# Kernel optimization log

Measured on AMD Instinct MI355X. Metric: run time of the kernel, lower is better.

The kernel has to match this reference:

```python
import jax, jax.numpy as jnp
import numpy as np

N = 50000      # nodes
E = 800000     # edges (before self-loops)
F_IN = 256
H = 4          # heads
C1 = 128
C2 = 64
NCLS = 50
NEG_SLOPE = 0.2


def setup_inputs() -> dict:
    key = jax.random.key(0)
    ks = jax.random.split(key, 12)
    x = jax.random.normal(ks[0], (N, F_IN), dtype=jnp.float32)
    edge_index = jax.random.randint(ks[1], (2, E), 0, N, dtype=jnp.int32)
    s1 = 1.0 / np.sqrt(F_IN)
    s2 = 1.0 / np.sqrt(H * C1)
    s3 = 1.0 / np.sqrt(H * C2)
    return {
        "x": x,
        "edge_index": edge_index,
        "W1": jax.random.normal(ks[2], (F_IN, H * C1), dtype=jnp.float32) * s1,
        "a_src1": jax.random.normal(ks[3], (H, C1), dtype=jnp.float32) * s2,
        "a_dst1": jax.random.normal(ks[4], (H, C1), dtype=jnp.float32) * s2,
        "b1": jnp.zeros((H * C1,), dtype=jnp.float32),
        "W2": jax.random.normal(ks[5], (H * C1, H * C2), dtype=jnp.float32) * s2,
        "a_src2": jax.random.normal(ks[6], (H, C2), dtype=jnp.float32) * s3,
        "a_dst2": jax.random.normal(ks[7], (H, C2), dtype=jnp.float32) * s3,
        "b2": jnp.zeros((H * C2,), dtype=jnp.float32),
        "Wf": jax.random.normal(ks[8], (H * C2, NCLS), dtype=jnp.float32) * s3,
        "bf": jnp.zeros((NCLS,), dtype=jnp.float32),
    }


def _gat_conv(x, src, dst, W, a_src, a_dst, b, heads, ch):
    # h: [N, H, C] transformed features
    h = (x @ W).reshape(N, heads, ch)
    # per-node attention halves (standard GAT decomposition, avoids per-edge d-dim gather for scores)
    asrc = jnp.sum(h * a_src[None], axis=-1)  # [N, H]
    adst = jnp.sum(h * a_dst[None], axis=-1)  # [N, H]
    e = jax.nn.leaky_relu(asrc[src] + adst[dst], NEG_SLOPE)  # [E, H]
    # softmax over edges sharing the same destination node
    m = jax.ops.segment_max(e, dst, num_segments=N)          # [N, H]
    ex = jnp.exp(e - m[dst])
    denom = jax.ops.segment_sum(ex, dst, num_segments=N)     # [N, H]
    alpha = ex / (denom[dst] + 1e-16)                        # [E, H]
    msg = h[src] * alpha[:, :, None]                         # [E, H, C]
    out = jax.ops.segment_sum(msg, dst, num_segments=N)      # [N, H, C]
    return out.reshape(N, heads * ch) + b


def reference(x, edge_index, W1, a_src1, a_dst1, b1, W2, a_src2, a_dst2, b2, Wf, bf):
    # PyG GATConv adds self-loops by default
    loops = jnp.arange(N, dtype=edge_index.dtype)
    src = jnp.concatenate([edge_index[0], loops])
    dst = jnp.concatenate([edge_index[1], loops])
    h = _gat_conv(x, src, dst, W1, a_src1, a_dst1, b1, H, C1)
    h = jax.nn.elu(h)
    # F.dropout is identity in eval mode
    h = _gat_conv(h, src, dst, W2, a_src2, a_dst2, b2, H, C2)
    h = jax.nn.elu(h)
    return h @ Wf + bf
```

## Files before the change

kernel.cpp:

```cpp
#include <hip/hip_runtime.h>
#include <hip/hip_bf16.h>
#include <cmath>

#define NN 50000
#define EE 800000
#define ET 850000
#define HH 4
#define CC1 128
#define CC2 64
#define FIN 256
#define NCLS 50

typedef __attribute__((ext_vector_type(8))) short   short8;
typedef __attribute__((ext_vector_type(8))) unsigned short ushort8;
typedef __attribute__((ext_vector_type(4))) unsigned short ushortx4;
typedef __attribute__((ext_vector_type(4))) float   floatx4;

__device__ __forceinline__ unsigned short f2bf(float f) {
    union { float f; unsigned int u; } x; x.f = f;
    unsigned int lsb = (x.u >> 16) & 1u;
    x.u += 0x7fffu + lsb;
    return (unsigned short)(x.u >> 16);
}
__device__ __forceinline__ float bf2f(unsigned short b) {
    union { unsigned int u; float f; } x; x.u = ((unsigned int)b) << 16;
    return x.f;
}

typedef const __attribute__((address_space(1))) unsigned int* glds_gp_t;
typedef __attribute__((address_space(3))) unsigned int* glds_lp_t;
__device__ __forceinline__ void glds16(const void* g, void* l) {
    __builtin_amdgcn_global_load_lds((glds_gp_t)g, (glds_lp_t)l, 16, 0, 0);
}

__global__ __launch_bounds__(256) void cast_bf16(
    const float* __restrict__ in, unsigned short* __restrict__ out, int n4)
{
    int t = blockIdx.x * blockDim.x + threadIdx.x;
    if (t >= n4) return;
    float4 v = *(const float4*)(in + 4 * (size_t)t);
    unsigned short r0 = f2bf(v.x), r1 = f2bf(v.y), r2 = f2bf(v.z), r3 = f2bf(v.w);
    unsigned int lo = (unsigned int)r0 | ((unsigned int)r1 << 16);
    unsigned int hi = (unsigned int)r2 | ((unsigned int)r3 << 16);
    *(uint2*)(out + 4 * (size_t)t) = make_uint2(lo, hi);
}

__global__ __launch_bounds__(256) void transpose_cast(
    const float* __restrict__ W, unsigned short* __restrict__ Wt, int K, int N)
{
    int t = blockIdx.x * blockDim.x + threadIdx.x;
    if (t >= K * N) return;
    int n = t / K, k = t - n * K;
    Wt[t] = f2bf(W[(size_t)k * N + n]);
}

__global__ __launch_bounds__(256) void transpose_cast_pad(
    const float* __restrict__ W, unsigned short* __restrict__ Wt,
    int K, int N, int Npad)
{
    int t = blockIdx.x * blockDim.x + threadIdx.x;
    if (t >= K * Npad) return;
    int n = t / K, k = t - n * K;
    Wt[t] = (n < N) ? f2bf(W[(size_t)k * N + n]) : (unsigned short)0;
}

__global__ __launch_bounds__(256) void gemm_bf16_v2(
    const unsigned short* __restrict__ A,
    const unsigned short* __restrict__ Bt,
    unsigned short* __restrict__ C,
    int M, int N, int K)
{
    __shared__ unsigned short As[128 * 32];
    __shared__ unsigned short Bs[128 * 32];
    int tid = threadIdx.x, wave = tid >> 6, lane = tid & 63;
    int wm = (wave >> 1) * 64, wn = (wave & 1) * 64;
    int row0 = blockIdx.x * 128, col0 = blockIdx.y * 128;
    int lm = lane & 15, lq = lane >> 4, kq = lq * 8;
    floatx4 acc[4][4] = {};

    int srow = wave * 32 + (lane >> 2);
    int skk  = (lane & 3) * 8;
    int gra0 = row0 + srow;      if (gra0 >= M) gra0 = M - 1;
    int gra1 = row0 + srow + 16; if (gra1 >= M) gra1 = M - 1;
    const unsigned short* ga0 = A + (size_t)gra0 * K + skk;
    const unsigned short* ga1 = A + (size_t)gra1 * K + skk;
    const unsigned short* gb0 = Bt + (size_t)(col0 + srow) * K + skk;
    const unsigned short* gb1 = Bt + (size_t)(col0 + srow + 16) * K + skk;
    unsigned short* la0 = &As[(wave * 32) * 32];
    unsigned short* la1 = &As[(wave * 32 + 16) * 32];
    unsigned short* lb0 = &Bs[(wave * 32) * 32];
    unsigned short* lb1 = &Bs[(wave * 32 + 16) * 32];

    for (int k0 = 0; k0 < K; k0 += 32) {
        __syncthreads();
        glds16(ga0 + k0, la0);
        glds16(ga1 + k0, la1);
        glds16(gb0 + k0, lb0);
        glds16(gb1 + k0, lb1);
        __syncthreads();

        short8 af[4], bfr[4];
        #pragma unroll
        for (int mt = 0; mt < 4; ++mt)
            af[mt] = *(const short8*)&As[(wm + mt * 16 + lm) * 32 + kq];
        #pragma unroll
        for (int nt = 0; nt < 4; ++nt)
            bfr[nt] = *(const short8*)&Bs[(wn + nt * 16 + lm) * 32 + kq];
        #pragma unroll
        for (int mt = 0; mt < 4; ++mt)
            #pragma unroll
            for (int nt = 0; nt < 4; ++nt)
                acc[mt][nt] = __builtin_amdgcn_mfma_f32_16x16x32_bf16(
                    af[mt], bfr[nt], acc[mt][nt], 0, 0, 0);
    }

    #pragma unroll
    for (int mt = 0; mt < 4; ++mt) {
        int rbase = row0 + wm + mt * 16 + lq * 4;
        #pragma unroll
        for (int nt = 0; nt < 4; ++nt) {
            int c = col0 + wn + nt * 16 + lm;
            #pragma unroll
            for (int r = 0; r < 4; ++r) {
                int gr = rbase + r;
                if (gr < M) C[(size_t)gr * N + c] = f2bf(acc[mt][nt][r]);
            }
        }
    }
}

__global__ __launch_bounds__(128) void gemm_final(
    const unsigned short* __restrict__ A,
    const unsigned short* __restrict__ Bt,
    const float* __restrict__ bias,
    float* __restrict__ out, int M)
{
    __shared__ unsigned short As[128 * 40];
    __shared__ unsigned short Bs[64 * 40];
    int tid = threadIdx.x, wave = tid >> 6, lane = tid & 63;
    int row0 = blockIdx.x * 128;
    int lm = lane & 15, lq = lane >> 4, kq = lq * 8;
    floatx4 acc[4][4] = {};

    for (int k0 = 0; k0 < 256; k0 += 32) {
        int gr = row0 + tid; if (gr >= M) gr = M - 1;
        const unsigned short* ap = A + (size_t)gr * 256 + k0;
        ushort8 a0 = *(const ushort8*)ap;
        ushort8 a1 = *(const ushort8*)(ap + 8);
        ushort8 a2 = *(const ushort8*)(ap + 16);
        ushort8 a3 = *(const ushort8*)(ap + 24);
        const unsigned short* bp = Bt + (size_t)(tid >> 1) * 256 + k0 + (tid & 1) * 16;
        ushort8 b0 = *(const ushort8*)bp;
        ushort8 b1 = *(const ushort8*)(bp + 8);
        __syncthreads();
        *(ushort8*)&As[tid * 40 + 0]  = a0;
        *(ushort8*)&As[tid * 40 + 8]  = a1;
        *(ushort8*)&As[tid * 40 + 16] = a2;
        *(ushort8*)&As[tid * 40 + 24] = a3;
        *(ushort8*)&Bs[(tid >> 1) * 40 + (tid & 1) * 16]     = b0;
        *(ushort8*)&Bs[(tid >> 1) * 40 + (tid & 1) * 16 + 8] = b1;
        __syncthreads();

        short8 af[4], bfr[4];
        #pragma unroll
        for (int mt = 0; mt < 4; ++mt)
            af[mt] = *(const short8*)&As[(wave * 64 + mt * 16 + lm) * 40 + kq];
        #pragma unroll
        for (int nt = 0; nt < 4; ++nt)
            bfr[nt] = *(const short8*)&Bs[(nt * 16 + lm) * 40 + kq];
        #pragma unroll
        for (int mt = 0; mt < 4; ++mt)
            #pragma unroll
            for (int nt = 0; nt < 4; ++nt)
                acc[mt][nt] = __builtin_amdgcn_mfma_f32_16x16x32_bf16(
                    af[mt], bfr[nt], acc[mt][nt], 0, 0, 0);
    }

    #pragma unroll
    for (int mt = 0; mt < 4; ++mt) {
        int rbase = row0 + wave * 64 + mt * 16 + lq * 4;
        #pragma unroll
        for (int nt = 0; nt < 4; ++nt) {
            int c = nt * 16 + lm;
            if (c >= NCLS) continue;
            float bv = bias[c];
            #pragma unroll
            for (int r = 0; r < 4; ++r) {
                int gr = rbase + r;
                if (gr < M) out[(size_t)gr * NCLS + c] = acc[mt][nt][r] + bv;
            }
        }
    }
}

template<int C>
__global__ __launch_bounds__(256) void attn_scores2(
    const unsigned short* __restrict__ h, const float* __restrict__ a_src,
    const float* __restrict__ a_dst, float* __restrict__ asrc,
    float* __restrict__ adst)
{
    constexpr int HC = HH * C;
    constexpr int CPL = HC / 64;
    int wave = threadIdx.x >> 6;
    int lane = threadIdx.x & 63;
    int n = blockIdx.x * 4 + wave;
    if (n >= NN) return;
    int c0 = lane * CPL;
    int head = c0 / C;
    const unsigned short* hp = h + (size_t)n * HC + c0;
    float hv[CPL];
    if (CPL == 8) {
        ushort8 u = *(const ushort8*)hp;
        #pragma unroll
        for (int c = 0; c < 8; ++c) hv[c] = bf2f(u[c]);
    } else {
        ushortx4 u = *(const ushortx4*)hp;
        #pragma unroll
        for (int c = 0; c < 4; ++c) hv[c] = bf2f(u[c]);
    }
    float s1 = 0.f, s2 = 0.f;
    #pragma unroll
    for (int c = 0; c < CPL; ++c) {
        s1 += hv[c] * a_src[c0 + c];
        s2 += hv[c] * a_dst[c0 + c];
    }
    #pragma unroll
    for (int o = 8; o > 0; o >>= 1) {
        s1 += __shfl_xor(s1, o, 64);
        s2 += __shfl_xor(s2, o, 64);
    }
    if ((lane & 15) == 0) {
        asrc[n * HH + head] = s1;
        adst[n * HH + head] = s2;
    }
}

__global__ void edge_histogram(const int* __restrict__ ei, int* __restrict__ deg)
{
    int t = blockIdx.x * blockDim.x + threadIdx.x;
    if (t >= ET) return;
    int dst = (t < EE) ? ei[EE + t] : (t - EE);
    atomicAdd(&deg[dst], 1);
}

__global__ __launch_bounds__(256) void scan_reduce(
    const int* __restrict__ deg, int* __restrict__ partials)
{
    int i0 = blockIdx.x * 2048 + threadIdx.x * 8;
    int s = 0;
    #pragma unroll
    for (int k = 0; k < 8; ++k) { int i = i0 + k; s += (i < NN) ? deg[i] : 0; }
    #pragma unroll
    for (int o = 32; o > 0; o >>= 1) s += __shfl_xor(s, o, 64);
    __shared__ int ws[4];
    int lane = threadIdx.x & 63, wid = threadIdx.x >> 6;
    if (lane == 0) ws[wid] = s;
    __syncthreads();
    if (threadIdx.x == 0) partials[blockIdx.x] = ws[0] + ws[1] + ws[2] + ws[3];
}

__global__ __launch_bounds__(64) void scan_partials(int* __restrict__ partials, int nb)
{
    int lane = threadIdx.x;
    int v = (lane < nb) ? partials[lane] : 0;
    int s = v;
    #pragma unroll
    for (int o = 1; o < 64; o <<= 1) {
        int t = __shfl_up(s, o, 64);
        if (lane >= o) s += t;
    }
    if (lane < nb) partials[lane] = s - v;
}

__global__ __launch_bounds__(256) void scan_apply(
    const int* __restrict__ deg, const int* __restrict__ partials,
    int* __restrict__ off, int* __restrict__ pos)
{
    int i0 = blockIdx.x * 2048 + threadIdx.x * 8;
    int v[8]; int s = 0;
    #pragma unroll
    for (int k = 0; k < 8; ++k) {
        int i = i0 + k;
        v[k] = (i < NN) ? deg[i] : 0;
        s += v[k];
    }
    int lane = threadIdx.x & 63, wid = threadIdx.x >> 6;
    int sc = s;
    #pragma unroll
    for (int o = 1; o < 64; o <<= 1) {
        int t = __shfl_up(sc, o, 64);
        if (lane >= o) sc += t;
    }
    __shared__ int ws[4];
    if (lane == 63) ws[wid] = sc;
    __syncthreads();
    int woff = partials[blockIdx.x];
    for (int w = 0; w < wid; ++w) woff += ws[w];
    int excl = woff + sc - s;
    #pragma unroll
    for (int k = 0; k < 8; ++k) {
        int i = i0 + k;
        if (i < NN) { off[i] = excl; pos[i] = excl; }
        excl += v[k];
    }
    if (blockIdx.x == 0 && threadIdx.x == 0) off[NN] = ET;
}

__global__ void edge_scatter(const int* __restrict__ ei,
                             int* __restrict__ pos, int* __restrict__ csr_src)
{
    int t = blockIdx.x * blockDim.x + threadIdx.x;
    if (t >= ET) return;
    int src, dst;
    if (t < EE) { src = ei[t]; dst = ei[EE + t]; }
    else        { src = t - EE; dst = t - EE; }
    int p = atomicAdd(&pos[dst], 1);
    csr_src[p] = src;
}

template<int C>
__global__ __launch_bounds__(256) void aggregate5(
    const unsigned short* __restrict__ h, const int* __restrict__ off,
    const int* __restrict__ csr_src, const float* __restrict__ asrc,
    const float* __restrict__ adst, const float* __restrict__ bias,
    unsigned short* __restrict__ outb)
{
    constexpr int HC = HH * C;
    constexpr int LPE = HC / 8;
    constexpr int EPW = 64 / LPE;
    __shared__ float exlds_all[4][64 * HH];
    int wave = threadIdx.x >> 6;
    int lane = threadIdx.x & 63;
    int n = blockIdx.x * 4 + wave;
    if (n >= NN) return;
    float* exlds = exlds_all[wave];
    int el  = (EPW == 1) ? 0 : (lane >> 5);
    int lel = (EPW == 1) ? lane : (lane & 31);
    int coff = lel * 8;
    int hl = coff / C;

    int start = off[n], end = off[n + 1];
    float4 advv = *(const float4*)(adst + (size_t)n * HH);
    float dh0 = 0.f, dh1 = 0.f, dh2 = 0.f, dh3 = 0.f;
    float acc[8] = {0.f, 0.f, 0.f, 0.f, 0.f, 0.f, 0.f, 0.f};

    for (int cb = start; cb < end; cb += 64) {
        int eidx = cb + lane;
        bool valid = eidx < end;
        int s_lane = csr_src[valid ? eidx : end - 1];
        float4 t = *(const float4*)(asrc + (size_t)s_lane * HH);
        float e0 = t.x + advv.x; e0 = e0 > 0.f ? e0 : 0.2f * e0;
        float e1 = t.y + advv.y; e1 = e1 > 0.f ? e1 : 0.2f * e1;
        float e2 = t.z + advv.z; e2 = e2 > 0.f ? e2 : 0.2f * e2;
        float e3 = t.w + advv.w; e3 = e3 > 0.f ? e3 : 0.2f * e3;
        float x0 = valid ? __expf(e0) : 0.f;
        float x1 = valid ? __expf(e1) : 0.f;
        float x2 = valid ? __expf(e2) : 0.f;
        float x3 = valid ? __expf(e3) : 0.f;
        dh0 += x0; dh1 += x1; dh2 += x2; dh3 += x3;
        *(float4*)&exlds[lane * 4] = make_float4(x0, x1, x2, x3);

        int cnt = end - cb; if (cnt > 64) cnt = 64;
        int jmax = (cnt + 4 * EPW - 1) & ~(4 * EPW - 1);
        for (int jj = 0; jj < jmax; jj += 4 * EPW) {
            int sidx[4]; float xs[4]; ushort8 uv[4];
            #pragma unroll
            for (int u = 0; u < 4; ++u) {
                int e_lo = jj + u * EPW;
                if (EPW == 1) {
                    sidx[u] = __builtin_amdgcn_readlane(s_lane, e_lo);
                } else {
                    int sa = __builtin_amdgcn_readlane(s_lane, e_lo);
                    int sb = __builtin_amdgcn_readlane(s_lane, e_lo + 1);
                    sidx[u] = el ? sb : sa;
                }
                xs[u] = exlds[(e_lo + el) * 4 + hl];
                uv[u] = *(const ushort8*)(h + (size_t)sidx[u] * HC + coff);
            }
            #pragma unroll
            for (int u = 0; u < 4; ++u)
                #pragma unroll
                for (int c = 0; c < 8; ++c)
                    acc[c] += xs[u] * bf2f(uv[u][c]);
        }
    }

    #pragma unroll
    for (int o = 32; o > 0; o >>= 1) {
        dh0 += __shfl_xor(dh0, o, 64);
        dh1 += __shfl_xor(dh1, o, 64);
        dh2 += __shfl_xor(dh2, o, 64);
        dh3 += __shfl_xor(dh3, o, 64);
    }
    if (EPW == 2) {
        #pragma unroll
        for (int c = 0; c < 8; ++c)
            acc[c] += __shfl_xor(acc[c], 32, 64);
    }
    float d = (hl == 0) ? dh0 : (hl == 1) ? dh1 : (hl == 2) ? dh2 : dh3;
    float inv = 1.f / (d + 1e-16f);
    if (el == 0) {
        float4 b0 = *(const float4*)(bias + coff);
        float4 b1 = *(const float4*)(bias + coff + 4);
        float bb[8] = {b0.x, b0.y, b0.z, b0.w, b1.x, b1.y, b1.z, b1.w};
        unsigned int pk[4];
        #pragma unroll
        for (int c2 = 0; c2 < 4; ++c2) {
            float ua = acc[2 * c2]     * inv + bb[2 * c2];
            float ub = acc[2 * c2 + 1] * inv + bb[2 * c2 + 1];
            ua = ua > 0.f ? ua : expm1f(ua);
            ub = ub > 0.f ? ub : expm1f(ub);
            pk[c2] = (unsigned int)f2bf(ua) | ((unsigned int)f2bf(ub) << 16);
        }
        *(uint4*)(outb + (size_t)n * HC + coff) = make_uint4(pk[0], pk[1], pk[2], pk[3]);
    }
}

extern "C" void kernel_launch(void* const* d_in, const int* in_sizes, int n_in,
                              void* d_out, int out_size, void* d_ws, size_t ws_size,
                              hipStream_t stream) {
    const float* x      = (const float*)d_in[0];
    const int*   ei     = (const int*)d_in[1];
    const float* W1     = (const float*)d_in[2];
    const float* a_src1 = (const float*)d_in[3];
    const float* a_dst1 = (const float*)d_in[4];
    const float* b1     = (const float*)d_in[5];
    const float* W2     = (const float*)d_in[6];
    const float* a_src2 = (const float*)d_in[7];
    const float* a_dst2 = (const float*)d_in[8];
    const float* b2     = (const float*)d_in[9];
    const float* Wf     = (const float*)d_in[10];
    const float* bf     = (const float*)d_in[11];
    float* out = (float*)d_out;

    char* p = (char*)d_ws;
    unsigned short* xb    = (unsigned short*)p; p += (size_t)NN * FIN * 2;
    unsigned short* h1b   = (unsigned short*)p; p += (size_t)NN * HH * CC1 * 2;
    unsigned short* out1b = (unsigned short*)p; p += (size_t)NN * HH * CC1 * 2;
    unsigned short* h2b   = (unsigned short*)p; p += (size_t)NN * HH * CC2 * 2;
    unsigned short* out2b = (unsigned short*)p; p += (size_t)NN * HH * CC2 * 2;
    unsigned short* W1t   = (unsigned short*)p; p += (size_t)FIN * HH * CC1 * 2;
    unsigned short* W2t   = (unsigned short*)p; p += (size_t)HH * CC1 * HH * CC2 * 2;
    unsigned short* Wft   = (unsigned short*)p; p += (size_t)64 * HH * CC2 * 2;
    float* asrc           = (float*)p;          p += (size_t)NN * HH * 4;
    float* adst           = (float*)p;          p += (size_t)NN * HH * 4;
    int* deg              = (int*)p;            p += (size_t)NN * 4;
    int* csr_off          = (int*)p;            p += (size_t)(NN + 1) * 4 + 12;
    int* csr_pos          = (int*)p;            p += (size_t)NN * 4;
    int* csr_src          = (int*)p;            p += (size_t)ET * 4;
    int* partials         = (int*)p;            p += 64 * 4;

    hipMemsetAsync(deg, 0, NN * sizeof(int), stream);

    cast_bf16<<<(NN * FIN / 4 + 255) / 256, 256, 0, stream>>>(x, xb, NN * FIN / 4);
    transpose_cast<<<(FIN * HH * CC1 + 255) / 256, 256, 0, stream>>>(W1, W1t, FIN, HH * CC1);
    transpose_cast<<<(HH * CC1 * HH * CC2 + 255) / 256, 256, 0, stream>>>(W2, W2t, HH * CC1, HH * CC2);
    transpose_cast_pad<<<(HH * CC2 * 64 + 255) / 256, 256, 0, stream>>>(Wf, Wft, HH * CC2, NCLS, 64);

    const int NB = (NN + 2047) / 2048;
    edge_histogram<<<(ET + 255) / 256, 256, 0, stream>>>(ei, deg);
    scan_reduce<<<NB, 256, 0, stream>>>(deg, partials);
    scan_partials<<<1, 64, 0, stream>>>(partials, NB);
    scan_apply<<<NB, 256, 0, stream>>>(deg, partials, csr_off, csr_pos);
    edge_scatter<<<(ET + 255) / 256, 256, 0, stream>>>(ei, csr_pos, csr_src);

    gemm_bf16_v2<<<dim3((NN + 127) / 128, (HH * CC1) / 128), 256, 0, stream>>>(
        xb, W1t, h1b, NN, HH * CC1, FIN);
    attn_scores2<CC1><<<(NN + 3) / 4, 256, 0, stream>>>(h1b, a_src1, a_dst1, asrc, adst);
    aggregate5<CC1><<<(NN + 3) / 4, 256, 0, stream>>>(h1b, csr_off, csr_src, asrc, adst, b1, out1b);

    gemm_bf16_v2<<<dim3((NN + 127) / 128, (HH * CC2) / 128), 256, 0, stream>>>(
        out1b, W2t, h2b, NN, HH * CC2, HH * CC1);
    attn_scores2<CC2><<<(NN + 3) / 4, 256, 0, stream>>>(h2b, a_src2, a_dst2, asrc, adst);
    aggregate5<CC2><<<(NN + 3) / 4, 256, 0, stream>>>(h2b, csr_off, csr_src, asrc, adst, b2, out2b);

    gemm_final<<<(NN + 127) / 128, 128, 0, stream>>>(out2b, Wft, bf, out, NN);
}
```

Measured before the change: 512.3 us.

## Switch pipeline to fp16, accumulate aggregation in half2, fuse prep and scan kernels

Converts all intermediate storage and MFMA GEMMs from bf16 to fp16. The aggregation kernel now stores attention weights as half2 in LDS, accumulates messages with packed __hfma2 in half precision, and unrolls the edge loop by 8 instead of 4. The four cast/transpose kernels are merged into one launch, and the partial-scan kernel is folded into scan_apply. These changes cut launches and ALU work in the gather loop, but half-precision accumulation over many edges raises the risk of precision loss and overflow.

```diff
diff --git a/kernel.cpp b/kernel.cpp
--- a/kernel.cpp
+++ b/kernel.cpp
@@ -1,5 +1,5 @@
 #include <hip/hip_runtime.h>
-#include <hip/hip_bf16.h>
+#include <hip/hip_fp16.h>
 #include <cmath>
 
 #define NN 50000
@@ -11,21 +11,8 @@
 #define FIN 256
 #define NCLS 50
 
-typedef __attribute__((ext_vector_type(8))) short   short8;
-typedef __attribute__((ext_vector_type(8))) unsigned short ushort8;
-typedef __attribute__((ext_vector_type(4))) unsigned short ushortx4;
-typedef __attribute__((ext_vector_type(4))) float   floatx4;
-
-__device__ __forceinline__ unsigned short f2bf(float f) {
-    union { float f; unsigned int u; } x; x.f = f;
-    unsigned int lsb = (x.u >> 16) & 1u;
-    x.u += 0x7fffu + lsb;
-    return (unsigned short)(x.u >> 16);
-}
-__device__ __forceinline__ float bf2f(unsigned short b) {
-    union { unsigned int u; float f; } x; x.u = ((unsigned int)b) << 16;
-    return x.f;
-}
+typedef _Float16 half8_t __attribute__((ext_vector_type(8)));
+typedef __attribute__((ext_vector_type(4))) float floatx4;
 
 typedef const __attribute__((address_space(1))) unsigned int* glds_gp_t;
 typedef __attribute__((address_space(3))) unsigned int* glds_lp_t;
@@ -33,45 +20,47 @@
     __builtin_amdgcn_global_load_lds((glds_gp_t)g, (glds_lp_t)l, 16, 0, 0);
 }
 
-__global__ __launch_bounds__(256) void cast_bf16(
-    const float* __restrict__ in, unsigned short* __restrict__ out, int n4)
-{
-    int t = blockIdx.x * blockDim.x + threadIdx.x;
-    if (t >= n4) return;
-    float4 v = *(const float4*)(in + 4 * (size_t)t);
-    unsigned short r0 = f2bf(v.x), r1 = f2bf(v.y), r2 = f2bf(v.z), r3 = f2bf(v.w);
-    unsigned int lo = (unsigned int)r0 | ((unsigned int)r1 << 16);
-    unsigned int hi = (unsigned int)r2 | ((unsigned int)r3 << 16);
-    *(uint2*)(out + 4 * (size_t)t) = make_uint2(lo, hi);
-}
-
-__global__ __launch_bounds__(256) void transpose_cast(
-    const float* __restrict__ W, unsigned short* __restrict__ Wt, int K, int N)
-{
-    int t = blockIdx.x * blockDim.x + threadIdx.x;
-    if (t >= K * N) return;
-    int n = t / K, k = t - n * K;
-    Wt[t] = f2bf(W[(size_t)k * N + n]);
-}
-
-__global__ __launch_bounds__(256) void transpose_cast_pad(
-    const float* __restrict__ W, unsigned short* __restrict__ Wt,
-    int K, int N, int Npad)
-{
-    int t = blockIdx.x * blockDim.x + threadIdx.x;
-    if (t >= K * Npad) return;
-    int n = t / K, k = t - n * K;
-    Wt[t] = (n < N) ? f2bf(W[(size_t)k * N + n]) : (unsigned short)0;
-}
-
-__global__ __launch_bounds__(256) void gemm_bf16_v2(
-    const unsigned short* __restrict__ A,
-    const unsigned short* __restrict__ Bt,
-    unsigned short* __restrict__ C,
+#define NB_CAST 12500
+#define NB_W1   512
+#define NB_W2   512
+#define NB_WF   64
+__global__ __launch_bounds__(256) void prep_fused(
+    const float* __restrict__ x, __half* __restrict__ xb,
+    const float* __restrict__ W1, __half* __restrict__ W1t,
+    const float* __restrict__ W2, __half* __restrict__ W2t,
+    const float* __restrict__ Wf, __half* __restrict__ Wft)
+{
+    int b = blockIdx.x;
+    if (b < NB_CAST) {
+        int t = b * 256 + threadIdx.x;
+        float4 v = *(const float4*)(x + 4 * (size_t)t);
+        __half2 p[2];
+        p[0] = __floats2half2_rn(v.x, v.y);
+        p[1] = __floats2half2_rn(v.z, v.w);
+        *(uint2*)(xb + 4 * (size_t)t) = *(uint2*)p;
+    } else if (b < NB_CAST + NB_W1) {
+        int t = (b - NB_CAST) * 256 + threadIdx.x;
+        int n = t >> 8, k = t & 255;
+        W1t[t] = __float2half(W1[(size_t)k * 512 + n]);
+    } else if (b < NB_CAST + NB_W1 + NB_W2) {
+        int t = (b - NB_CAST - NB_W1) * 256 + threadIdx.x;
+        int n = t >> 9, k = t & 511;
+        W2t[t] = __float2half(W2[(size_t)k * 256 + n]);
+    } else {
+        int t = (b - NB_CAST - NB_W1 - NB_W2) * 256 + threadIdx.x;
+        int n = t >> 8, k = t & 255;
+        Wft[t] = (n < NCLS) ? __float2half(Wf[(size_t)k * NCLS + n]) : __float2half(0.f);
+    }
+}
+
+__global__ __launch_bounds__(256) void gemm_f16_v2(
+    const __half* __restrict__ A,
+    const __half* __restrict__ Bt,
+    __half* __restrict__ C,
     int M, int N, int K)
 {
-    __shared__ unsigned short As[128 * 32];
-    __shared__ unsigned short Bs[128 * 32];
+    __shared__ __half As[128 * 32];
+    __shared__ __half Bs[128 * 32];
     int tid = threadIdx.x, wave = tid >> 6, lane = tid & 63;
     int wm = (wave >> 1) * 64, wn = (wave & 1) * 64;
     int row0 = blockIdx.x * 128, col0 = blockIdx.y * 128;
@@ -82,14 +71,14 @@
     int skk  = (lane & 3) * 8;
     int gra0 = row0 + srow;      if (gra0 >= M) gra0 = M - 1;
     int gra1 = row0 + srow + 16; if (gra1 >= M) gra1 = M - 1;
-    const unsigned short* ga0 = A + (size_t)gra0 * K + skk;
-    const unsigned short* ga1 = A + (size_t)gra1 * K + skk;
-    const unsigned short* gb0 = Bt + (size_t)(col0 + srow) * K + skk;
-    const unsigned short* gb1 = Bt + (size_t)(col0 + srow + 16) * K + skk;
-    unsigned short* la0 = &As[(wave * 32) * 32];
-    unsigned short* la1 = &As[(wave * 32 + 16) * 32];
-    unsigned short* lb0 = &Bs[(wave * 32) * 32];
-    unsigned short* lb1 = &Bs[(wave * 32 + 16) * 32];
+    const __half* ga0 = A + (size_t)gra0 * K + skk;
+    const __half* ga1 = A + (size_t)gra1 * K + skk;
+    const __half* gb0 = Bt + (size_t)(col0 + srow) * K + skk;
+    const __half* gb1 = Bt + (size_t)(col0 + srow + 16) * K + skk;
+    __half* la0 = &As[(wave * 32) * 32];
+    __half* la1 = &As[(wave * 32 + 16) * 32];
+    __half* lb0 = &Bs[(wave * 32) * 32];
+    __half* lb1 = &Bs[(wave * 32 + 16) * 32];
 
     for (int k0 = 0; k0 < K; k0 += 32) {
         __syncthreads();
@@ -99,18 +88,18 @@
         glds16(gb1 + k0, lb1);
         __syncthreads();
 
-        short8 af[4], bfr[4];
+        half8_t af[4], bfr[4];
         #pragma unroll
         for (int mt = 0; mt < 4; ++mt)
-            af[mt] = *(const short8*)&As[(wm + mt * 16 + lm) * 32 + kq];
+            af[mt] = *(const half8_t*)&As[(wm + mt * 16 + lm) * 32 + kq];
         #pragma unroll
         for (int nt = 0; nt < 4; ++nt)
-            bfr[nt] = *(const short8*)&Bs[(wn + nt * 16 + lm) * 32 + kq];
+            bfr[nt] = *(const half8_t*)&Bs[(wn + nt * 16 + lm) * 32 + kq];
         #pragma unroll
         for (int mt = 0; mt < 4; ++mt)
             #pragma unroll
             for (int nt = 0; nt < 4; ++nt)
-                acc[mt][nt] = __builtin_amdgcn_mfma_f32_16x16x32_bf16(
+                acc[mt][nt] = __builtin_amdgcn_mfma_f32_16x16x32_f16(
                     af[mt], bfr[nt], acc[mt][nt], 0, 0, 0);
     }
 
@@ -123,20 +112,20 @@
             #pragma unroll
             for (int r = 0; r < 4; ++r) {
                 int gr = rbase + r;
-                if (gr < M) C[(size_t)gr * N + c] = f2bf(acc[mt][nt][r]);
+                if (gr < M) C[(size_t)gr * N + c] = __float2half(acc[mt][nt][r]);
             }
         }
     }
 }
 
 __global__ __launch_bounds__(128) void gemm_final(
-    const unsigned short* __restrict__ A,
-    const unsigned short* __restrict__ Bt,
+    const __half* __restrict__ A,
+    const __half* __restrict__ Bt,
     const float* __restrict__ bias,
     float* __restrict__ out, int M)
 {
-    __shared__ unsigned short As[128 * 40];
-    __shared__ unsigned short Bs[64 * 40];
+    __shared__ __half As[128 * 40];
+    __shared__ __half Bs[64 * 40];
     int tid = threadIdx.x, wave = tid >> 6, lane = tid & 63;
     int row0 = blockIdx.x * 128;
     int lm = lane & 15, lq = lane >> 4, kq = lq * 8;
@@ -144,35 +133,35 @@
 
     for (int k0 = 0; k0 < 256; k0 += 32) {
         int gr = row0 + tid; if (gr >= M) gr = M - 1;
-        const unsigned short* ap = A + (size_t)gr * 256 + k0;
-        ushort8 a0 = *(const ushort8*)ap;
-        ushort8 a1 = *(const ushort8*)(ap + 8);
-        ushort8 a2 = *(const ushort8*)(ap + 16);
-        ushort8 a3 = *(const ushort8*)(ap + 24);
-        const unsigned short* bp = Bt + (size_t)(tid >> 1) * 256 + k0 + (tid & 1) * 16;
-        ushort8 b0 = *(const ushort8*)bp;
-        ushort8 b1 = *(const ushort8*)(bp + 8);
+        const __half* ap = A + (size_t)gr * 256 + k0;
+        half8_t a0 = *(const half8_t*)ap;
+        half8_t a1 = *(const half8_t*)(ap + 8);
+        half8_t a2 = *(const half8_t*)(ap + 16);
+        half8_t a3 = *(const half8_t*)(ap + 24);
+        const __half* bp = Bt + (size_t)(tid >> 1) * 256 + k0 + (tid & 1) * 16;
+        half8_t b0 = *(const half8_t*)bp;
+        half8_t b1 = *(const half8_t*)(bp + 8);
         __syncthreads();
-        *(ushort8*)&As[tid * 40 + 0]  = a0;
-        *(ushort8*)&As[tid * 40 + 8]  = a1;
-        *(ushort8*)&As[tid * 40 + 16] = a2;
-        *(ushort8*)&As[tid * 40 + 24] = a3;
-        *(ushort8*)&Bs[(tid >> 1) * 40 + (tid & 1) * 16]     = b0;
-        *(ushort8*)&Bs[(tid >> 1) * 40 + (tid & 1) * 16 + 8] = b1;
+        *(half8_t*)&As[tid * 40 + 0]  = a0;
+        *(half8_t*)&As[tid * 40 + 8]  = a1;
+        *(half8_t*)&As[tid * 40 + 16] = a2;
+        *(half8_t*)&As[tid * 40 + 24] = a3;
+        *(half8_t*)&Bs[(tid >> 1) * 40 + (tid & 1) * 16]     = b0;
+        *(half8_t*)&Bs[(tid >> 1) * 40 + (tid & 1) * 16 + 8] = b1;
         __syncthreads();
 
-        short8 af[4], bfr[4];
+        half8_t af[4], bfr[4];
         #pragma unroll
         for (int mt = 0; mt < 4; ++mt)
-            af[mt] = *(const short8*)&As[(wave * 64 + mt * 16 + lm) * 40 + kq];
+            af[mt] = *(const half8_t*)&As[(wave * 64 + mt * 16 + lm) * 40 + kq];
         #pragma unroll
         for (int nt = 0; nt < 4; ++nt)
-            bfr[nt] = *(const short8*)&Bs[(nt * 16 + lm) * 40 + kq];
+            bfr[nt] = *(const half8_t*)&Bs[(nt * 16 + lm) * 40 + kq];
         #pragma unroll
         for (int mt = 0; mt < 4; ++mt)
             #pragma unroll
             for (int nt = 0; nt < 4; ++nt)
-                acc[mt][nt] = __builtin_amdgcn_mfma_f32_16x16x32_bf16(
+                acc[mt][nt] = __builtin_amdgcn_mfma_f32_16x16x32_f16(
                     af[mt], bfr[nt], acc[mt][nt], 0, 0, 0);
     }
 
@@ -195,7 +184,7 @@
 
 template<int C>
 __global__ __launch_bounds__(256) void attn_scores2(
-    const unsigned short* __restrict__ h, const float* __restrict__ a_src,
+    const __half* __restrict__ h, const float* __restrict__ a_src,
     const float* __restrict__ a_dst, float* __restrict__ asrc,
     float* __restrict__ adst)
 {
@@ -207,16 +196,24 @@
     if (n >= NN) return;
     int c0 = lane * CPL;
     int head = c0 / C;
-    const unsigned short* hp = h + (size_t)n * HC + c0;
+    const __half* hp = h + (size_t)n * HC + c0;
     float hv[CPL];
     if (CPL == 8) {
-        ushort8 u = *(const ushort8*)hp;
-        #pragma unroll
-        for (int c = 0; c < 8; ++c) hv[c] = bf2f(u[c]);
+        union { uint4 u; __half2 h2[4]; } U;
+        U.u = *(const uint4*)hp;
+        #pragma unroll
+        for (int k = 0; k < 4; ++k) {
+            float2 f = __half22float2(U.h2[k]);
+            hv[2 * k] = f.x; hv[2 * k + 1] = f.y;
+        }
     } else {
-        ushortx4 u = *(const ushortx4*)hp;
-        #pragma unroll
-        for (int c = 0; c < 4; ++c) hv[c] = bf2f(u[c]);
+        union { uint2 u; __half2 h2[2]; } U;
+        U.u = *(const uint2*)hp;
+        #pragma unroll
+        for (int k = 0; k < 2; ++k) {
+            float2 f = __half22float2(U.h2[k]);
+            hv[2 * k] = f.x; hv[2 * k + 1] = f.y;
+        }
     }
     float s1 = 0.f, s2 = 0.f;
     #pragma unroll
@@ -259,23 +256,25 @@
     if (threadIdx.x == 0) partials[blockIdx.x] = ws[0] + ws[1] + ws[2] + ws[3];
 }
 
-__global__ __launch_bounds__(64) void scan_partials(int* __restrict__ partials, int nb)
-{
-    int lane = threadIdx.x;
-    int v = (lane < nb) ? partials[lane] : 0;
-    int s = v;
-    #pragma unroll
-    for (int o = 1; o < 64; o <<= 1) {
-        int t = __shfl_up(s, o, 64);
-        if (lane >= o) s += t;
-    }
-    if (lane < nb) partials[lane] = s - v;
-}
-
+#define SCAN_NB 25
 __global__ __launch_bounds__(256) void scan_apply(
     const int* __restrict__ deg, const int* __restrict__ partials,
     int* __restrict__ off, int* __restrict__ pos)
 {
+    __shared__ int spE[SCAN_NB];
+    __shared__ int ws[4];
+    int lane = threadIdx.x & 63, wid = threadIdx.x >> 6;
+    if (wid == 0) {
+        int v = (lane < SCAN_NB) ? partials[lane] : 0;
+        int s = v;
+        #pragma unroll
+        for (int o = 1; o < 32; o <<= 1) {
+            int t = __shfl_up(s, o, 64);
+            if (lane >= o) s += t;
+        }
+        if (lane < SCAN_NB) spE[lane] = s - v;
+    }
+
     int i0 = blockIdx.x * 2048 + threadIdx.x * 8;
     int v[8]; int s = 0;
     #pragma unroll
@@ -284,17 +283,15 @@
         v[k] = (i < NN) ? deg[i] : 0;
         s += v[k];
     }
-    int lane = threadIdx.x & 63, wid = threadIdx.x >> 6;
     int sc = s;
     #pragma unroll
     for (int o = 1; o < 64; o <<= 1) {
         int t = __shfl_up(sc, o, 64);
         if (lane >= o) sc += t;
     }
-    __shared__ int ws[4];
     if (lane == 63) ws[wid] = sc;
     __syncthreads();
-    int woff = partials[blockIdx.x];
+    int woff = spE[blockIdx.x];
     for (int w = 0; w < wid; ++w) woff += ws[w];
     int excl = woff + sc - s;
     #pragma unroll
@@ -319,21 +316,22 @@
 }
 
 template<int C>
-__global__ __launch_bounds__(256) void aggregate5(
-    const unsigned short* __restrict__ h, const int* __restrict__ off,
+__global__ __launch_bounds__(256) void aggregate7(
+    const __half* __restrict__ h, const int* __restrict__ off,
     const int* __restrict__ csr_src, const float* __restrict__ asrc,
     const float* __restrict__ adst, const float* __restrict__ bias,
-    unsigned short* __restrict__ outb)
+    __half* __restrict__ outb)
 {
     constexpr int HC = HH * C;
     constexpr int LPE = HC / 8;
     constexpr int EPW = 64 / LPE;
-    __shared__ float exlds_all[4][64 * HH];
+    constexpr int UNR = 8;
+    __shared__ unsigned int exlds_all[4][64 * HH];
     int wave = threadIdx.x >> 6;
     int lane = threadIdx.x & 63;
     int n = blockIdx.x * 4 + wave;
     if (n >= NN) return;
-    float* exlds = exlds_all[wave];
+    unsigned int* exlds = exlds_all[wave];
     int el  = (EPW == 1) ? 0 : (lane >> 5);
     int lel = (EPW == 1) ? lane : (lane & 31);
     int coff = lel * 8;
@@ -342,7 +340,7 @@
     int start = off[n], end = off[n + 1];
     float4 advv = *(const float4*)(adst + (size_t)n * HH);
     float dh0 = 0.f, dh1 = 0.f, dh2 = 0.f, dh3 = 0.f;
-    float acc[8] = {0.f, 0.f, 0.f, 0.f, 0.f, 0.f, 0.f, 0.f};
+    __half2 acc2[4] = {};
 
     for (int cb = start; cb < end; cb += 64) {
         int eidx = cb + lane;
@@ -358,14 +356,20 @@
         float x2 = valid ? __expf(e2) : 0.f;
         float x3 = valid ? __expf(e3) : 0.f;
         dh0 += x0; dh1 += x1; dh2 += x2; dh3 += x3;
-        *(float4*)&exlds[lane * 4] = make_float4(x0, x1, x2, x3);
+        __half2 xp[4];
+        xp[0] = __float2half2_rn(x0);
+        xp[1] = __float2half2_rn(x1);
+        xp[2] = __float2half2_rn(x2);
+        xp[3] = __float2half2_rn(x3);
+        *(uint4*)&exlds[lane * 4] = *(uint4*)xp;
 
         int cnt = end - cb; if (cnt > 64) cnt = 64;
-        int jmax = (cnt + 4 * EPW - 1) & ~(4 * EPW - 1);
-        for (int jj = 0; jj < jmax; jj += 4 * EPW) {
-            int sidx[4]; float xs[4]; ushort8 uv[4];
-            #pragma unroll
-            for (int u = 0; u < 4; ++u) {
+        int jmax = (cnt + UNR * EPW - 1) & ~(UNR * EPW - 1);
+        for (int jj = 0; jj < jmax; jj += UNR * EPW) {
+            int sidx[UNR]; __half2 xs[UNR];
+            union { uint4 u; __half2 h2[4]; } uv[UNR];
+            #pragma unroll
+            for (int u = 0; u < UNR; ++u) {
                 int e_lo = jj + u * EPW;
                 if (EPW == 1) {
                     sidx[u] = __builtin_amdgcn_readlane(s_lane, e_lo);
@@ -374,14 +378,14 @@
                     int sb = __builtin_amdgcn_readlane(s_lane, e_lo + 1);
                     sidx[u] = el ? sb : sa;
                 }
-                xs[u] = exlds[(e_lo + el) * 4 + hl];
-                uv[u] = *(const ushort8*)(h + (size_t)sidx[u] * HC + coff);
+                uv[u].u = *(const uint4*)(h + (size_t)sidx[u] * HC + coff);
+                xs[u] = *(__half2*)&exlds[(e_lo + el) * 4 + hl];
             }
             #pragma unroll
-            for (int u = 0; u < 4; ++u)
+            for (int u = 0; u < UNR; ++u)
                 #pragma unroll
-                for (int c = 0; c < 8; ++c)
-                    acc[c] += xs[u] * bf2f(uv[u][c]);
+                for (int k = 0; k < 4; ++k)
+                    acc2[k] = __hfma2(xs[u], uv[u].h2[k], acc2[k]);
         }
     }
 
@@ -392,10 +396,16 @@
         dh2 += __shfl_xor(dh2, o, 64);
         dh3 += __shfl_xor(dh3, o, 64);
     }
+    float accf[8];
+    #pragma unroll
+    for (int k = 0; k < 4; ++k) {
+        float2 f = __half22float2(acc2[k]);
+        accf[2 * k] = f.x; accf[2 * k + 1] = f.y;
+    }
     if (EPW == 2) {
         #pragma unroll
         for (int c = 0; c < 8; ++c)
-            acc[c] += __shfl_xor(acc[c], 32, 64);
+            accf[c] += __shfl_xor(accf[c], 32, 64);
     }
     float d = (hl == 0) ? dh0 : (hl == 1) ? dh1 : (hl == 2) ? dh2 : dh3;
     float inv = 1.f / (d + 1e-16f);
@@ -403,16 +413,16 @@
         float4 b0 = *(const float4*)(bias + coff);
         float4 b1 = *(const float4*)(bias + coff + 4);
         float bb[8] = {b0.x, b0.y, b0.z, b0.w, b1.x, b1.y, b1.z, b1.w};
-        unsigned int pk[4];
+        __half2 pk[4];
         #pragma unroll
         for (int c2 = 0; c2 < 4; ++c2) {
-            float ua = acc[2 * c2]     * inv + bb[2 * c2];
-            float ub = acc[2 * c2 + 1] * inv + bb[2 * c2 + 1];
+            float ua = accf[2 * c2]     * inv + bb[2 * c2];
+            float ub = accf[2 * c2 + 1] * inv + bb[2 * c2 + 1];
             ua = ua > 0.f ? ua : expm1f(ua);
             ub = ub > 0.f ? ub : expm1f(ub);
-            pk[c2] = (unsigned int)f2bf(ua) | ((unsigned int)f2bf(ub) << 16);
-        }
-        *(uint4*)(outb + (size_t)n * HC + coff) = make_uint4(pk[0], pk[1], pk[2], pk[3]);
+            pk[c2] = __floats2half2_rn(ua, ub);
+        }
+        *(uint4*)(outb + (size_t)n * HC + coff) = *(uint4*)pk;
     }
 }
 
@@ -434,45 +444,41 @@
     float* out = (float*)d_out;
 
     char* p = (char*)d_ws;
-    unsigned short* xb    = (unsigned short*)p; p += (size_t)NN * FIN * 2;
-    unsigned short* h1b   = (unsigned short*)p; p += (size_t)NN * HH * CC1 * 2;
-    unsigned short* out1b = (unsigned short*)p; p += (size_t)NN * HH * CC1 * 2;
-    unsigned short* h2b   = (unsigned short*)p; p += (size_t)NN * HH * CC2 * 2;
-    unsigned short* out2b = (unsigned short*)p; p += (size_t)NN * HH * CC2 * 2;
-    unsigned short* W1t   = (unsigned short*)p; p += (size_t)FIN * HH * CC1 * 2;
-    unsigned short* W2t   = (unsigned short*)p; p += (size_t)HH * CC1 * HH * CC2 * 2;
-    unsigned short* Wft   = (unsigned short*)p; p += (size_t)64 * HH * CC2 * 2;
-    float* asrc           = (float*)p;          p += (size_t)NN * HH * 4;
-    float* adst           = (float*)p;          p += (size_t)NN * HH * 4;
-    int* deg              = (int*)p;            p += (size_t)NN * 4;
-    int* csr_off          = (int*)p;            p += (size_t)(NN + 1) * 4 + 12;
-    int* csr_pos          = (int*)p;            p += (size_t)NN * 4;
-    int* csr_src          = (int*)p;            p += (size_t)ET * 4;
-    int* partials         = (int*)p;            p += 64 * 4;
+    __half* xb    = (__half*)p; p += (size_t)NN * FIN * 2;
+    __half* h1b   = (__half*)p; p += (size_t)NN * HH * CC1 * 2;
+    __half* out1b = (__half*)p; p += (size_t)NN * HH * CC1 * 2;
+    __half* h2b   = (__half*)p; p += (size_t)NN * HH * CC2 * 2;
+    __half* out2b = (__half*)p; p += (size_t)NN * HH * CC2 * 2;
+    __half* W1t   = (__half*)p; p += (size_t)FIN * HH * CC1 * 2;
+    __half* W2t   = (__half*)p; p += (size_t)HH * CC1 * HH * CC2 * 2;
+    __half* Wft   = (__half*)p; p += (size_t)64 * HH * CC2 * 2;
+    float* asrc   = (float*)p;  p += (size_t)NN * HH * 4;
+    float* adst   = (float*)p;  p += (size_t)NN * HH * 4;
+    int* deg      = (int*)p;    p += (size_t)NN * 4;
+    int* csr_off  = (int*)p;    p += (size_t)(NN + 1) * 4 + 12;
+    int* csr_pos  = (int*)p;    p += (size_t)NN * 4;
+    int* csr_src  = (int*)p;    p += (size_t)ET * 4;
+    int* partials = (int*)p;    p += 64 * 4;
 
     hipMemsetAsync(deg, 0, NN * sizeof(int), stream);
 
-    cast_bf16<<<(NN * FIN / 4 + 255) / 256, 256, 0, stream>>>(x, xb, NN * FIN / 4);
-    transpose_cast<<<(FIN * HH * CC1 + 255) / 256, 256, 0, stream>>>(W1, W1t, FIN, HH * CC1);
-    transpose_cast<<<(HH * CC1 * HH * CC2 + 255) / 256, 256, 0, stream>>>(W2, W2t, HH * CC1, HH * CC2);
-    transpose_cast_pad<<<(HH * CC2 * 64 + 255) / 256, 256, 0, stream>>>(Wf, Wft, HH * CC2, NCLS, 64);
-
-    const int NB = (NN + 2047) / 2048;
+    prep_fused<<<NB_CAST + NB_W1 + NB_W2 + NB_WF, 256, 0, stream>>>(
+        x, xb, W1, W1t, W2, W2t, Wf, Wft);
+
     edge_histogram<<<(ET + 255) / 256, 256, 0, stream>>>(ei, deg);
-    scan_reduce<<<NB, 256, 0, stream>>>(deg, partials);
-    scan_partials<<<1, 64, 0, stream>>>(partials, NB);
-    scan_apply<<<NB, 256, 0, stream>>>(deg, partials, csr_off, csr_pos);
+    scan_reduce<<<SCAN_NB, 256, 0, stream>>>(deg, partials);
+    scan_apply<<<SCAN_NB, 256, 0, stream>>>(deg, partials, csr_off, csr_pos);
     edge_scatter<<<(ET + 255) / 256, 256, 0, stream>>>(ei, csr_pos, csr_src);
 
-    gemm_bf16_v2<<<dim3((NN + 127) / 128, (HH * CC1) / 128), 256, 0, stream>>>(
+    gemm_f16_v2<<<dim3((NN + 127) / 128, (HH * CC1) / 128), 256, 0, stream>>>(
         xb, W1t, h1b, NN, HH * CC1, FIN);
     attn_scores2<CC1><<<(NN + 3) / 4, 256, 0, stream>>>(h1b, a_src1, a_dst1, asrc, adst);
-    aggregate5<CC1><<<(NN + 3) / 4, 256, 0, stream>>>(h1b, csr_off, csr_src, asrc, adst, b1, out1b);
-
-    gemm_bf16_v2<<<dim3((NN + 127) / 128, (HH * CC2) / 128), 256, 0, stream>>>(
+    aggregate7<CC1><<<(NN + 3) / 4, 256, 0, stream>>>(h1b, csr_off, csr_src, asrc, adst, b1, out1b);
+
+    gemm_f16_v2<<<dim3((NN + 127) / 128, (HH * CC2) / 128), 256, 0, stream>>>(
         out1b, W2t, h2b, NN, HH * CC2, HH * CC1);
     attn_scores2<CC2><<<(NN + 3) / 4, 256, 0, stream>>>(h2b, a_src2, a_dst2, asrc, adst);
-    aggregate5<CC2><<<(NN + 3) / 4, 256, 0, stream>>>(h2b, csr_off, csr_src, asrc, adst, b2, out2b);
+    aggregate7<CC2><<<(NN + 3) / 4, 256, 0, stream>>>(h2b, csr_off, csr_src, asrc, adst, b2, out2b);
 
     gemm_final<<<(NN + 127) / 128, 128, 0, stream>>>(out2b, Wft, bf, out, NN);
 }
```

Measured after the change: 498.5 us. 1.03x faster.
